# Optimization experiments

Hardware: AMD Instinct MI355X
Metric: run time of the kernel (lower is better)

The kernel has to match this reference:

```python
import jax, jax.numpy as jnp
import numpy as np

B, T, C, H = 2, 2048, 512, 8
HD = C // H  # head size = 64

def _layernorm(x, g, b, eps=1e-5):
    mu = jnp.mean(x, axis=-1, keepdims=True)
    var = jnp.var(x, axis=-1, keepdims=True)
    return (x - mu) * jax.lax.rsqrt(var + eps) * g + b

def setup_inputs() -> dict:
    key = jax.random.key(0)
    ks = jax.random.split(key, 12)
    s_attn = 1.0 / np.sqrt(C)
    s_proj = 1.0 / np.sqrt(H * HD)
    s_ffn1 = 1.0 / np.sqrt(C)
    s_ffn2 = 1.0 / np.sqrt(4 * C)
    return {
        "x":   jax.random.normal(ks[0], (B, T, C), jnp.float32),
        "Wq":  jax.random.uniform(ks[1], (H, C, HD), jnp.float32, -s_attn, s_attn),
        "Wk":  jax.random.uniform(ks[2], (H, C, HD), jnp.float32, -s_attn, s_attn),
        "Wv":  jax.random.uniform(ks[3], (H, C, HD), jnp.float32, -s_attn, s_attn),
        "Wo":  jax.random.uniform(ks[4], (H * HD, C), jnp.float32, -s_proj, s_proj),
        "bo":  jax.random.uniform(ks[5], (C,), jnp.float32, -s_proj, s_proj),
        "W1":  jax.random.uniform(ks[6], (C, 4 * C), jnp.float32, -s_ffn1, s_ffn1),
        "b1":  jax.random.uniform(ks[7], (4 * C,), jnp.float32, -s_ffn1, s_ffn1),
        "W2":  jax.random.uniform(ks[8], (4 * C, C), jnp.float32, -s_ffn2, s_ffn2),
        "b2":  jax.random.uniform(ks[9], (C,), jnp.float32, -s_ffn2, s_ffn2),
        "g1":  jnp.ones((C,), jnp.float32),
        "be1": jnp.zeros((C,), jnp.float32),
        "g2":  jnp.ones((C,), jnp.float32),
        "be2": jnp.zeros((C,), jnp.float32),
    }

def reference(x, Wq, Wk, Wv, Wo, bo, W1, b1, W2, b2, g1, be1, g2, be2):
    # --- multi-head causal self-attention on ln1(x) ---
    h = _layernorm(x, g1, be1)
    q = jnp.einsum("btc,hcd->bhtd", h, Wq)
    k = jnp.einsum("btc,hcd->bhtd", h, Wk)
    v = jnp.einsum("btc,hcd->bhtd", h, Wv)
    scores = jnp.einsum("bhtd,bhsd->bhts", q, k) * (HD ** -0.5)
    causal = jnp.tril(jnp.ones((T, T), bool))
    scores = jnp.where(causal, scores, -jnp.inf)
    wei = jax.nn.softmax(scores, axis=-1)
    attn = jnp.einsum("bhts,bhsd->bhtd", wei, v)
    attn = attn.transpose(0, 2, 1, 3).reshape(B, T, H * HD)  # concat heads
    x = x + attn @ Wo + bo
    # --- GELU MLP on ln2(x) ---
    h2 = _layernorm(x, g2, be2)
    ff = jax.nn.gelu(h2 @ W1 + b1, approximate=False) @ W2 + b2
    return x + ff
```

## Files before the change

### kernel.cpp

```cpp
#include <hip/hip_runtime.h>
#include <math.h>

constexpr int B_   = 2;
constexpr int T_   = 2048;
constexpr int C_   = 512;
constexpr int H_   = 8;
constexpr int HD_  = 64;
constexpr int M_   = B_ * T_;
constexpr int FF_  = 4 * C_;
constexpr int NQKV_ = 3 * C_;

typedef __attribute__((ext_vector_type(8))) short short8;
typedef __attribute__((ext_vector_type(4))) short short4v;
typedef __attribute__((ext_vector_type(4))) float floatx4;

static __device__ __forceinline__ unsigned short f2bf(float f) {
    union { float f; unsigned u; } v; v.f = f;
    unsigned r = v.u + 0x7fff + ((v.u >> 16) & 1);
    return (unsigned short)(r >> 16);
}

static __device__ __forceinline__ unsigned packbf2(float a, float b) {
    union { float f; unsigned u; } x, y; x.f = a; y.f = b;
    unsigned lo = (x.u + 0x7fff + ((x.u >> 16) & 1)) >> 16;
    unsigned hi = (y.u + 0x7fff + ((y.u >> 16) & 1)) & 0xffff0000u;
    return lo | hi;
}

static __device__ __forceinline__ void gl2lds16(const unsigned short* g,
                                                unsigned short* l) {
    __builtin_amdgcn_global_load_lds(
        (const __attribute__((address_space(1))) void*)g,
        (__attribute__((address_space(3))) void*)l, 16, 0, 0);
}

#if __has_builtin(__builtin_amdgcn_mfma_f32_16x16x16bf16_1k)
static __device__ __forceinline__ floatx4 mfma16(short4v a, short4v b, floatx4 c) {
    return __builtin_amdgcn_mfma_f32_16x16x16bf16_1k(a, b, c, 0, 0, 0);
}
#elif __has_builtin(__builtin_amdgcn_mfma_f32_16x16x16_bf16)
static __device__ __forceinline__ floatx4 mfma16(short4v a, short4v b, floatx4 c) {
    return __builtin_amdgcn_mfma_f32_16x16x16_bf16(a, b, c, 0, 0, 0);
}
#else
static __device__ __forceinline__ floatx4 mfma16(short4v a, short4v b, floatx4 c) {
    asm volatile("v_mfma_f32_16x16x16_bf16 %0, %1, %2, %0"
                 : "+v"(c) : "v"(a), "v"(b));
    return c;
}
#endif

__global__ void prep_weights(const float* __restrict__ Wq,
                             const float* __restrict__ Wk,
                             const float* __restrict__ Wv,
                             const float* __restrict__ Wo,
                             const float* __restrict__ W1,
                             const float* __restrict__ W2,
                             unsigned short* __restrict__ Wqkv_t,
                             unsigned short* __restrict__ Wo_t,
                             unsigned short* __restrict__ W1_t,
                             unsigned short* __restrict__ W2_t) {
    __shared__ float tile[32][33];
    int idx = blockIdx.x;
    const float* src; unsigned short* dst;
    int K, N, k0, n0;
    float scale = 1.0f;
    if (idx < 768) {
        int wz = idx >> 8, rem = idx & 255;
        int h = rem >> 5, r2 = rem & 31;
        k0 = (r2 >> 1) * 32; n0 = (r2 & 1) * 32;
        src = (wz == 0 ? Wq : (wz == 1 ? Wk : Wv)) + (size_t)h * C_ * HD_;
        dst = Wqkv_t + (size_t)(wz * C_ + h * HD_) * C_;
        K = C_; N = HD_;
        if (wz == 0) scale = 0.125f;
    } else if (idx < 1024) {
        int rem = idx - 768;
        n0 = (rem & 15) * 32; k0 = (rem >> 4) * 32;
        src = Wo; dst = Wo_t; K = C_; N = C_;
    } else if (idx < 2048) {
        int rem = idx - 1024;
        n0 = (rem & 63) * 32; k0 = (rem >> 6) * 32;
        src = W1; dst = W1_t; K = C_; N = FF_;
    } else {
        int rem = idx - 2048;
        n0 = (rem & 15) * 32; k0 = (rem >> 4) * 32;
        src = W2; dst = W2_t; K = FF_; N = C_;
    }
    int tx = threadIdx.x, ty = threadIdx.y;
#pragma unroll
    for (int i = 0; i < 4; i++)
        tile[ty + i * 8][tx] = src[(size_t)(k0 + ty + i * 8) * N + n0 + tx];
    __syncthreads();
#pragma unroll
    for (int i = 0; i < 4; i++)
        dst[(size_t)(n0 + ty + i * 8) * K + k0 + tx] = f2bf(tile[tx][ty + i * 8] * scale);
}

__global__ void v_transpose(const unsigned short* __restrict__ qkv,
                            unsigned short* __restrict__ vT) {
    __shared__ unsigned short tile[32][33];
    int bh = blockIdx.z, b = bh >> 3, h = bh & 7;
    int t0 = blockIdx.x * 32, d0 = blockIdx.y * 32;
    int tx = threadIdx.x, ty = threadIdx.y;
#pragma unroll
    for (int i = 0; i < 4; i++)
        tile[ty + i * 8][tx] = qkv[(size_t)(b * T_ + t0 + ty + i * 8) * NQKV_
                                   + 2 * C_ + h * HD_ + d0 + tx];
    __syncthreads();
#pragma unroll
    for (int i = 0; i < 4; i++)
        vT[(size_t)(bh * HD_ + d0 + ty + i * 8) * T_ + t0 + tx] = tile[tx][ty + i * 8];
}

__global__ void ln_kernel(const float* __restrict__ x,
                          const float* __restrict__ g,
                          const float* __restrict__ b,
                          unsigned short* __restrict__ out) {
    int row  = blockIdx.x;
    int lane = threadIdx.x;
    const float* xr = x + (size_t)row * C_;
    int c0 = lane * 8;
    float4 v0 = *(const float4*)(xr + c0);
    float4 v1 = *(const float4*)(xr + c0 + 4);
    float vals[8] = {v0.x, v0.y, v0.z, v0.w, v1.x, v1.y, v1.z, v1.w};

    float s = 0.f, ss = 0.f;
#pragma unroll
    for (int j = 0; j < 8; j++) { s += vals[j]; ss += vals[j] * vals[j]; }
#pragma unroll
    for (int off = 32; off; off >>= 1) {
        s  += __shfl_xor(s,  off);
        ss += __shfl_xor(ss, off);
    }
    float mu  = s / C_;
    float var = ss / C_ - mu * mu;
    float rs  = rsqrtf(var + 1e-5f);

    unsigned short* orow = out + (size_t)row * C_;
#pragma unroll
    for (int j = 0; j < 8; j++) {
        int c = c0 + j;
        orow[c] = f2bf((vals[j] - mu) * rs * g[c] + b[c]);
    }
}

template<int BM, int BN, int BK>
__global__ __launch_bounds__(256) void mfma_gemm(
        const unsigned short* __restrict__ A,
        const unsigned short* __restrict__ Bt,
        const float* __restrict__ bias,
        const float* __restrict__ resid,
        float* __restrict__ outF,
        unsigned short* __restrict__ outB,
        int M, int N, int K, int flags) {
    constexpr int WM = BM / 2, WN = BN / 2;
    constexpr int MI = WM / 16, NI = WN / 16, KH = BK / 32;
    __shared__ unsigned short As[KH * BM * 32];
    __shared__ unsigned short Bs[KH * BN * 32];

    int t = threadIdx.x;
    int lane = t & 63, w = t >> 6;
    int wr = (w >> 1) * WM, wc = (w & 1) * WN;
    int lm = lane & 15, lq = lane >> 4;
    int m0 = blockIdx.y * BM, n0 = blockIdx.x * BN;

    floatx4 acc[MI][NI];
#pragma unroll
    for (int mi = 0; mi < MI; mi++)
#pragma unroll
        for (int ni = 0; ni < NI; ni++) acc[mi][ni] = (floatx4){0.f, 0.f, 0.f, 0.f};

    for (int k0 = 0; k0 < K; k0 += BK) {
        __syncthreads();
#pragma unroll
        for (int hh = 0; hh < KH; hh++) {
#pragma unroll
            for (int j = 0; j < BM * 4 / 256; j++) {
                int i = t + j * 256;
                gl2lds16(A + (size_t)(m0 + (i >> 2)) * K + k0 + hh * 32 + (i & 3) * 8,
                         &As[hh * BM * 32 + i * 8]);
            }
#pragma unroll
            for (int j = 0; j < BN * 4 / 256; j++) {
                int i = t + j * 256;
                gl2lds16(Bt + (size_t)(n0 + (i >> 2)) * K + k0 + hh * 32 + (i & 3) * 8,
                         &Bs[hh * BN * 32 + i * 8]);
            }
        }
        __syncthreads();

#pragma unroll
        for (int hh = 0; hh < KH; hh++) {
            short8 af[MI], bfv[NI];
#pragma unroll
            for (int mi = 0; mi < MI; mi++)
                af[mi] = *(const short8*)&As[hh * BM * 32 + (wr + mi * 16 + lm) * 32 + lq * 8];
#pragma unroll
            for (int ni = 0; ni < NI; ni++)
                bfv[ni] = *(const short8*)&Bs[hh * BN * 32 + (wc + ni * 16 + lm) * 32 + lq * 8];
#pragma unroll
            for (int mi = 0; mi < MI; mi++)
#pragma unroll
                for (int ni = 0; ni < NI; ni++)
                    acc[mi][ni] = __builtin_amdgcn_mfma_f32_16x16x32_bf16(
                        af[mi], bfv[ni], acc[mi][ni], 0, 0, 0);
        }
    }

#pragma unroll
    for (int mi = 0; mi < MI; mi++)
#pragma unroll
        for (int ni = 0; ni < NI; ni++) {
            int gc = n0 + wc + ni * 16 + lm;
#pragma unroll
            for (int r = 0; r < 4; r++) {
                int gr = m0 + wr + mi * 16 + lq * 4 + r;
                float v = acc[mi][ni][r];
                if (flags & 1) v += bias[gc];
                if (flags & 4) v = 0.5f * v * (1.0f + erff(v * 0.70710678118654752f));
                if (flags & 2) v += resid[(size_t)gr * N + gc];
                if (flags & 8) outB[(size_t)gr * N + gc] = f2bf(v);
                else           outF[(size_t)gr * N + gc] = v;
            }
        }
}

__global__ __launch_bounds__(256, 2) void attn_mfma(
        const unsigned short* __restrict__ qkv,
        const unsigned short* __restrict__ vT,
        unsigned short* __restrict__ o) {
    __shared__ unsigned short Ks[2][64 * 72];
    __shared__ unsigned short Vt[2][64 * 72];

    int t = threadIdx.x;
    int wq = t >> 6, lane = t & 63;
    int lm = lane & 15, quad = lane >> 4;
    int bh = blockIdx.y, b = bh >> 3, h = bh & 7;
    int x = blockIdx.x;
    int tile = (bh < 8) ? (2 * (x & 15) + (x >> 4))
                        : (2 * (x & 15) + 1 - (x >> 4));
    int q0 = tile * 64;

    int srow = t >> 2, sq4 = t & 3;

    const unsigned short* kbase = qkv + (size_t)(b * T_) * NQKV_ + C_ + h * HD_;
    const unsigned short* vbase = vT + (size_t)(bh * HD_ + srow) * T_;

    int gq_row = q0 + wq * 16 + lm;
    const unsigned short* qp = qkv + (size_t)(b * T_ + gq_row) * NQKV_ + h * HD_;
    short8 qf0 = *(const short8*)(qp + quad * 8);
    short8 qf1 = *(const short8*)(qp + 32 + quad * 8);

    float l_s = 0.f;
    floatx4 o_acc[4];
#pragma unroll
    for (int dt = 0; dt < 4; dt++) o_acc[dt] = (floatx4){0.f, 0.f, 0.f, 0.f};

    int nch = tile + 1;

    const unsigned short* kg = kbase + (size_t)srow * NQKV_ + sq4 * 16;
    short8 kp0 = *(const short8*)kg;
    short8 kp1 = *(const short8*)(kg + 8);
    short8 vp0 = *(const short8*)(vbase + sq4 * 16);
    short8 vp1 = *(const short8*)(vbase + sq4 * 16 + 8);
    *(short8*)&Ks[0][srow * 72 + sq4 * 16]     = kp0;
    *(short8*)&Ks[0][srow * 72 + sq4 * 16 + 8] = kp1;
    *(short8*)&Vt[0][srow * 72 + sq4 * 16]     = vp0;
    *(short8*)&Vt[0][srow * 72 + sq4 * 16 + 8] = vp1;

    for (int c = 0; c < nch; c++) {
        int buf = c & 1;
        if (c + 1 < nch) {
            int s0n = (c + 1) * 64;
            const unsigned short* kgn = kbase + (size_t)(s0n + srow) * NQKV_ + sq4 * 16;
            kp0 = *(const short8*)kgn;
            kp1 = *(const short8*)(kgn + 8);
            vp0 = *(const short8*)(vbase + s0n + sq4 * 16);
            vp1 = *(const short8*)(vbase + s0n + sq4 * 16 + 8);
        }
        __syncthreads();

        bool diag = (c == nch - 1);
#pragma unroll
        for (int kt = 0; kt < 4; kt++) {
            if (diag && kt > wq) continue;
            short8 kf0 = *(const short8*)&Ks[buf][(kt * 16 + lm) * 72 + quad * 8];
            short8 kf1 = *(const short8*)&Ks[buf][(kt * 16 + lm) * 72 + 32 + quad * 8];
            floatx4 s = (floatx4){0.f, 0.f, 0.f, 0.f};
            s = __builtin_amdgcn_mfma_f32_16x16x32_bf16(kf0, qf0, s, 0, 0, 0);
            s = __builtin_amdgcn_mfma_f32_16x16x32_bf16(kf1, qf1, s, 0, 0, 0);
            float p0, p1, p2, p3;
            {
                bool e = diag && (kt == wq);
                p0 = (e && (quad * 4 + 0 > lm)) ? 0.f : __expf(s[0]);
                p1 = (e && (quad * 4 + 1 > lm)) ? 0.f : __expf(s[1]);
                p2 = (e && (quad * 4 + 2 > lm)) ? 0.f : __expf(s[2]);
                p3 = (e && (quad * 4 + 3 > lm)) ? 0.f : __expf(s[3]);
            }
            l_s += (p0 + p1) + (p2 + p3);
            uint2 pu;
            pu.x = packbf2(p0, p1);
            pu.y = packbf2(p2, p3);
            short4v pk = *(short4v*)&pu;
#pragma unroll
            for (int dt = 0; dt < 4; dt++) {
                short4v vf = *(const short4v*)&Vt[buf][(dt * 16 + lm) * 72 + kt * 16 + quad * 4];
                o_acc[dt] = mfma16(pk, vf, o_acc[dt]);
            }
        }
        if (c + 1 < nch) {
            int nb = buf ^ 1;
            *(short8*)&Ks[nb][srow * 72 + sq4 * 16]     = kp0;
            *(short8*)&Ks[nb][srow * 72 + sq4 * 16 + 8] = kp1;
            *(short8*)&Vt[nb][srow * 72 + sq4 * 16]     = vp0;
            *(short8*)&Vt[nb][srow * 72 + sq4 * 16 + 8] = vp1;
        }
    }

    float lsum = l_s;
    lsum += __shfl_xor(lsum, 16);
    lsum += __shfl_xor(lsum, 32);
    float inv = 1.f / lsum;
#pragma unroll
    for (int r = 0; r < 4; r++) {
        float invq = __shfl(inv, quad * 4 + r);
        int gq = q0 + wq * 16 + quad * 4 + r;
        unsigned short* op = o + (size_t)(b * T_ + gq) * C_ + h * HD_ + lm;
#pragma unroll
        for (int dt = 0; dt < 4; dt++)
            op[dt * 16] = f2bf(o_acc[dt][r] * invq);
    }
}

extern "C" void kernel_launch(void* const* d_in, const int* in_sizes, int n_in,
                              void* d_out, int out_size, void* d_ws, size_t ws_size,
                              hipStream_t stream) {
    const float* x   = (const float*)d_in[0];
    const float* Wq  = (const float*)d_in[1];
    const float* Wk  = (const float*)d_in[2];
    const float* Wv  = (const float*)d_in[3];
    const float* Wo  = (const float*)d_in[4];
    const float* bo  = (const float*)d_in[5];
    const float* W1  = (const float*)d_in[6];
    const float* b1  = (const float*)d_in[7];
    const float* W2  = (const float*)d_in[8];
    const float* b2  = (const float*)d_in[9];
    const float* g1  = (const float*)d_in[10];
    const float* be1 = (const float*)d_in[11];
    const float* g2  = (const float*)d_in[12];
    const float* be2 = (const float*)d_in[13];
    float* out = (float*)d_out;

    unsigned short* Wqkv_t = (unsigned short*)d_ws;
    unsigned short* Wo_t   = Wqkv_t + (size_t)NQKV_ * C_;
    unsigned short* W1_t   = Wo_t   + (size_t)C_ * C_;
    unsigned short* W2_t   = W1_t   + (size_t)C_ * FF_;
    unsigned short* hb     = W2_t   + (size_t)FF_ * C_;
    unsigned short* attnb  = hb     + (size_t)M_ * C_;
    unsigned short* qkvb   = attnb  + (size_t)M_ * C_;
    unsigned short* vTb    = qkvb   + (size_t)M_ * NQKV_;
    unsigned short* ff1    = attnb;

    prep_weights<<<3072, dim3(32, 8), 0, stream>>>(
        Wq, Wk, Wv, Wo, W1, W2, Wqkv_t, Wo_t, W1_t, W2_t);

    ln_kernel<<<M_, 64, 0, stream>>>(x, g1, be1, hb);

    mfma_gemm<64, 128, 64><<<dim3(NQKV_ / 128, M_ / 64), 256, 0, stream>>>(
        hb, Wqkv_t, nullptr, nullptr, nullptr, qkvb, M_, NQKV_, C_, 8);

    v_transpose<<<dim3(T_ / 32, HD_ / 32, B_ * H_), dim3(32, 8), 0, stream>>>(
        qkvb, vTb);

    attn_mfma<<<dim3(32, B_ * H_), 256, 0, stream>>>(qkvb, vTb, attnb);

    mfma_gemm<64, 64, 64><<<dim3(C_ / 64, M_ / 64), 256, 0, stream>>>(
        attnb, Wo_t, bo, x, out, nullptr, M_, C_, C_, 1 | 2);

    ln_kernel<<<M_, 64, 0, stream>>>(out, g2, be2, hb);

    mfma_gemm<128, 128, 64><<<dim3(FF_ / 128, M_ / 128), 256, 0, stream>>>(
        hb, W1_t, b1, nullptr, nullptr, ff1, M_, FF_, C_, 1 | 4 | 8);

    mfma_gemm<64, 64, 64><<<dim3(C_ / 64, M_ / 64), 256, 0, stream>>>(
        ff1, W2_t, b2, out, out, nullptr, M_, C_, FF_, 1 | 2);
}
```

Measured before the change: 237.3 us.

## Split attention KV range across two blocks and combine partials

The attention kernel now splits each query tile's key chunks between two blocks using interleaved even and odd chunks. Each block writes unnormalized fp32 partial outputs and row sums, and a new combine kernel adds them, normalizes, and converts to bf16. This doubles the attention grid to 1024 blocks to improve occupancy on the many-CU GPU, and the launch bound is raised to 4. The cost is an extra kernel launch and fp32 partial traffic. The FFN1 GEMM tile is also reduced to 64x128 to create more blocks.

```diff
diff --git a/kernel.cpp b/kernel.cpp
--- a/kernel.cpp
+++ b/kernel.cpp
@@ -225,10 +225,11 @@
         }
 }
 
-__global__ __launch_bounds__(256, 2) void attn_mfma(
+__global__ __launch_bounds__(256, 4) void attn_mfma(
         const unsigned short* __restrict__ qkv,
         const unsigned short* __restrict__ vT,
-        unsigned short* __restrict__ o) {
+        float* __restrict__ oP,
+        float* __restrict__ lP) {
     __shared__ unsigned short Ks[2][64 * 72];
     __shared__ unsigned short Vt[2][64 * 72];
 
@@ -236,9 +237,7 @@
     int wq = t >> 6, lane = t & 63;
     int lm = lane & 15, quad = lane >> 4;
     int bh = blockIdx.y, b = bh >> 3, h = bh & 7;
-    int x = blockIdx.x;
-    int tile = (bh < 8) ? (2 * (x & 15) + (x >> 4))
-                        : (2 * (x & 15) + 1 - (x >> 4));
+    int tile = blockIdx.x >> 1, s = blockIdx.x & 1;
     int q0 = tile * 64;
 
     int srow = t >> 2, sq4 = t & 3;
@@ -256,22 +255,25 @@
 #pragma unroll
     for (int dt = 0; dt < 4; dt++) o_acc[dt] = (floatx4){0.f, 0.f, 0.f, 0.f};
 
-    int nch = tile + 1;
-
-    const unsigned short* kg = kbase + (size_t)srow * NQKV_ + sq4 * 16;
-    short8 kp0 = *(const short8*)kg;
-    short8 kp1 = *(const short8*)(kg + 8);
-    short8 vp0 = *(const short8*)(vbase + sq4 * 16);
-    short8 vp1 = *(const short8*)(vbase + sq4 * 16 + 8);
-    *(short8*)&Ks[0][srow * 72 + sq4 * 16]     = kp0;
-    *(short8*)&Ks[0][srow * 72 + sq4 * 16 + 8] = kp1;
-    *(short8*)&Vt[0][srow * 72 + sq4 * 16]     = vp0;
-    *(short8*)&Vt[0][srow * 72 + sq4 * 16 + 8] = vp1;
-
-    for (int c = 0; c < nch; c++) {
-        int buf = c & 1;
-        if (c + 1 < nch) {
-            int s0n = (c + 1) * 64;
+    short8 kp0, kp1, vp0, vp1;
+    if (s <= tile) {
+        int s0 = s * 64;
+        const unsigned short* kg = kbase + (size_t)(s0 + srow) * NQKV_ + sq4 * 16;
+        kp0 = *(const short8*)kg;
+        kp1 = *(const short8*)(kg + 8);
+        vp0 = *(const short8*)(vbase + s0 + sq4 * 16);
+        vp1 = *(const short8*)(vbase + s0 + sq4 * 16 + 8);
+        *(short8*)&Ks[0][srow * 72 + sq4 * 16]     = kp0;
+        *(short8*)&Ks[0][srow * 72 + sq4 * 16 + 8] = kp1;
+        *(short8*)&Vt[0][srow * 72 + sq4 * 16]     = vp0;
+        *(short8*)&Vt[0][srow * 72 + sq4 * 16 + 8] = vp1;
+    }
+
+    int buf = 0;
+    for (int c = s; c <= tile; c += 2) {
+        bool havenext = (c + 2 <= tile);
+        if (havenext) {
+            int s0n = (c + 2) * 64;
             const unsigned short* kgn = kbase + (size_t)(s0n + srow) * NQKV_ + sq4 * 16;
             kp0 = *(const short8*)kgn;
             kp1 = *(const short8*)(kgn + 8);
@@ -280,22 +282,22 @@
         }
         __syncthreads();
 
-        bool diag = (c == nch - 1);
+        bool diag = (c == tile);
 #pragma unroll
         for (int kt = 0; kt < 4; kt++) {
             if (diag && kt > wq) continue;
             short8 kf0 = *(const short8*)&Ks[buf][(kt * 16 + lm) * 72 + quad * 8];
             short8 kf1 = *(const short8*)&Ks[buf][(kt * 16 + lm) * 72 + 32 + quad * 8];
-            floatx4 s = (floatx4){0.f, 0.f, 0.f, 0.f};
-            s = __builtin_amdgcn_mfma_f32_16x16x32_bf16(kf0, qf0, s, 0, 0, 0);
-            s = __builtin_amdgcn_mfma_f32_16x16x32_bf16(kf1, qf1, s, 0, 0, 0);
+            floatx4 sv = (floatx4){0.f, 0.f, 0.f, 0.f};
+            sv = __builtin_amdgcn_mfma_f32_16x16x32_bf16(kf0, qf0, sv, 0, 0, 0);
+            sv = __builtin_amdgcn_mfma_f32_16x16x32_bf16(kf1, qf1, sv, 0, 0, 0);
             float p0, p1, p2, p3;
             {
                 bool e = diag && (kt == wq);
-                p0 = (e && (quad * 4 + 0 > lm)) ? 0.f : __expf(s[0]);
-                p1 = (e && (quad * 4 + 1 > lm)) ? 0.f : __expf(s[1]);
-                p2 = (e && (quad * 4 + 2 > lm)) ? 0.f : __expf(s[2]);
-                p3 = (e && (quad * 4 + 3 > lm)) ? 0.f : __expf(s[3]);
+                p0 = (e && (quad * 4 + 0 > lm)) ? 0.f : __expf(sv[0]);
+                p1 = (e && (quad * 4 + 1 > lm)) ? 0.f : __expf(sv[1]);
+                p2 = (e && (quad * 4 + 2 > lm)) ? 0.f : __expf(sv[2]);
+                p3 = (e && (quad * 4 + 3 > lm)) ? 0.f : __expf(sv[3]);
             }
             l_s += (p0 + p1) + (p2 + p3);
             uint2 pu;
@@ -308,28 +310,57 @@
                 o_acc[dt] = mfma16(pk, vf, o_acc[dt]);
             }
         }
-        if (c + 1 < nch) {
+        if (havenext) {
             int nb = buf ^ 1;
             *(short8*)&Ks[nb][srow * 72 + sq4 * 16]     = kp0;
             *(short8*)&Ks[nb][srow * 72 + sq4 * 16 + 8] = kp1;
             *(short8*)&Vt[nb][srow * 72 + sq4 * 16]     = vp0;
             *(short8*)&Vt[nb][srow * 72 + sq4 * 16 + 8] = vp1;
         }
+        buf ^= 1;
     }
 
     float lsum = l_s;
     lsum += __shfl_xor(lsum, 16);
     lsum += __shfl_xor(lsum, 32);
-    float inv = 1.f / lsum;
+    if (quad == 0)
+        lP[(size_t)s * M_ * H_ + (size_t)(b * T_ + q0 + wq * 16 + lm) * H_ + h] = lsum;
+    float* obase = oP + (size_t)s * M_ * C_;
 #pragma unroll
     for (int r = 0; r < 4; r++) {
-        float invq = __shfl(inv, quad * 4 + r);
         int gq = q0 + wq * 16 + quad * 4 + r;
-        unsigned short* op = o + (size_t)(b * T_ + gq) * C_ + h * HD_ + lm;
+        float* op = obase + (size_t)(b * T_ + gq) * C_ + h * HD_ + lm;
 #pragma unroll
         for (int dt = 0; dt < 4; dt++)
-            op[dt * 16] = f2bf(o_acc[dt][r] * invq);
-    }
+            op[dt * 16] = o_acc[dt][r];
+    }
+}
+
+__global__ void attn_combine(const float* __restrict__ oP,
+                             const float* __restrict__ lP,
+                             unsigned short* __restrict__ o) {
+    int row = blockIdx.x * 4 + (threadIdx.x >> 6);
+    int lane = threadIdx.x & 63;
+    int h = lane >> 3;
+    float l0 = lP[(size_t)row * H_ + h];
+    float l1 = lP[(size_t)M_ * H_ + (size_t)row * H_ + h];
+    float inv = 1.f / (l0 + l1);
+    int c0 = lane * 8;
+    const float* p0 = oP + (size_t)row * C_ + c0;
+    const float* p1 = oP + (size_t)M_ * C_ + (size_t)row * C_ + c0;
+    unsigned short* op = o + (size_t)row * C_ + c0;
+    float4 a0 = *(const float4*)p0;
+    float4 a1 = *(const float4*)(p0 + 4);
+    float4 b0 = *(const float4*)p1;
+    float4 b1 = *(const float4*)(p1 + 4);
+    op[0] = f2bf((a0.x + b0.x) * inv);
+    op[1] = f2bf((a0.y + b0.y) * inv);
+    op[2] = f2bf((a0.z + b0.z) * inv);
+    op[3] = f2bf((a0.w + b0.w) * inv);
+    op[4] = f2bf((a1.x + b1.x) * inv);
+    op[5] = f2bf((a1.y + b1.y) * inv);
+    op[6] = f2bf((a1.z + b1.z) * inv);
+    op[7] = f2bf((a1.w + b1.w) * inv);
 }
 
 extern "C" void kernel_launch(void* const* d_in, const int* in_sizes, int n_in,
@@ -359,6 +390,8 @@
     unsigned short* attnb  = hb     + (size_t)M_ * C_;
     unsigned short* qkvb   = attnb  + (size_t)M_ * C_;
     unsigned short* vTb    = qkvb   + (size_t)M_ * NQKV_;
+    float*          oPf    = (float*)(vTb + (size_t)M_ * C_);
+    float*          lPf    = oPf + 2 * (size_t)M_ * C_;
     unsigned short* ff1    = attnb;
 
     prep_weights<<<3072, dim3(32, 8), 0, stream>>>(
@@ -372,14 +405,16 @@
     v_transpose<<<dim3(T_ / 32, HD_ / 32, B_ * H_), dim3(32, 8), 0, stream>>>(
         qkvb, vTb);
 
-    attn_mfma<<<dim3(32, B_ * H_), 256, 0, stream>>>(qkvb, vTb, attnb);
+    attn_mfma<<<dim3(64, B_ * H_), 256, 0, stream>>>(qkvb, vTb, oPf, lPf);
+
+    attn_combine<<<M_ / 4, 256, 0, stream>>>(oPf, lPf, attnb);
 
     mfma_gemm<64, 64, 64><<<dim3(C_ / 64, M_ / 64), 256, 0, stream>>>(
         attnb, Wo_t, bo, x, out, nullptr, M_, C_, C_, 1 | 2);
 
     ln_kernel<<<M_, 64, 0, stream>>>(out, g2, be2, hb);
 
-    mfma_gemm<128, 128, 64><<<dim3(FF_ / 128, M_ / 128), 256, 0, stream>>>(
+    mfma_gemm<64, 128, 64><<<dim3(FF_ / 128, M_ / 64), 256, 0, stream>>>(
         hb, W1_t, b1, nullptr, nullptr, ff1, M_, FF_, C_, 1 | 4 | 8);
 
     mfma_gemm<64, 64, 64><<<dim3(C_ / 64, M_ / 64), 256, 0, stream>>>(
```

New measurement: 225.1 us. 5.2% less time.
